# Kernel tuning notes

Measured on AMD Instinct MI355X. Metric: run time of the kernel, lower is better.

Reference implementation:

```python
import jax, jax.numpy as jnp
import numpy as np

IN_F = 512
OUT_F = 512
GRID_SIZE = 5
SPLINE_ORDER = 3
BATCH = 16384
GRID_MIN, GRID_MAX = -1.0, 1.0


def setup_inputs() -> dict:
    key = jax.random.key(0)
    k1, k2, k3 = jax.random.split(key, 3)
    x = jax.random.normal(k1, (BATCH, IN_F), dtype=jnp.float32)
    # kaiming-uniform-ish scale for base weight
    base_weight = jax.random.normal(k2, (OUT_F, IN_F), dtype=jnp.float32) * (1.0 / np.sqrt(IN_F))
    spline_weight = jax.random.normal(k3, (OUT_F, IN_F, GRID_SIZE + SPLINE_ORDER), dtype=jnp.float32) * 0.1
    spline_scaler = jnp.ones((OUT_F, IN_F), dtype=jnp.float32)  # init'd to scale_spline=1.0
    # grid buffer: (in_features, grid_size + 2*spline_order + 1)
    h = (GRID_MAX - GRID_MIN) / GRID_SIZE
    knots = jnp.arange(-SPLINE_ORDER, GRID_SIZE + SPLINE_ORDER + 1, dtype=jnp.float32) * h + GRID_MIN
    grid = jnp.broadcast_to(knots, (IN_F, GRID_SIZE + 2 * SPLINE_ORDER + 1))
    return {"x": x, "base_weight": base_weight, "spline_weight": spline_weight,
            "spline_scaler": spline_scaler, "grid": grid}


def _b_splines(x, grid):
    # x: (B, in), grid: (in, G + 2k + 1) -> bases: (B, in, G + k)
    xe = x[..., None]  # (B, in, 1)
    bases = ((xe >= grid[:, :-1]) & (xe < grid[:, 1:])).astype(x.dtype)
    for k in range(1, SPLINE_ORDER + 1):
        den1 = jnp.maximum(grid[:, k:-1] - grid[:, :-(k + 1)], 1e-6)
        den2 = jnp.maximum(grid[:, k + 1:] - grid[:, 1:-k], 1e-6)
        bases = ((xe - grid[:, :-(k + 1)]) / den1 * bases[..., :-1]
                 + (grid[:, k + 1:] - xe) / den2 * bases[..., 1:])
    return bases


def reference(x, base_weight, spline_weight, spline_scaler, grid):
    # _finite: nan_to_num + clamp to [-6, 6]
    x = jnp.clip(jnp.nan_to_num(x, nan=0.0, posinf=6.0, neginf=-6.0), -6.0, 6.0)
    # clamp to slightly outside grid range, then (identity-like) renormalize
    x = jnp.clip(x, GRID_MIN - 0.1, GRID_MAX + 0.1)
    x = (x - GRID_MIN) / (GRID_MAX - GRID_MIN + 1e-8) * (GRID_MAX - GRID_MIN) + GRID_MIN
    base_out = jax.nn.silu(x) @ base_weight.T  # (B, out)
    bases = _b_splines(x, grid)                # (B, in, G+k)
    scaled_sw = spline_weight * spline_scaler[..., None]  # (out, in, G+k)
    spline_out = jnp.einsum('big,oig->bo', bases, scaled_sw)
    y = base_out + spline_out
    return jnp.where(jnp.isfinite(y), y, jnp.zeros_like(y))
```

## Files before the change

kernel.cpp:

```cpp
#include <hip/hip_runtime.h>
#include <stdint.h>


#define IN_F   512
#define OUT_F  512
#define KDIM   4608
#define BATCH  16384

#define BM 128
#define BN 128
#define BKI 128
#define NT (KDIM / BKI)
#define A_I8 (BM * BKI)
#define TILE_I8 (2 * A_I8)

#define SSCALE 154.0f
#define BSCALE 190.5f

typedef unsigned char u8;
typedef int i32x4 __attribute__((ext_vector_type(4)));

__device__ __forceinline__ float cleanx(float v) {
    if (v != v) v = 0.0f;
    v = fminf(fmaxf(v, -6.0f), 6.0f);
    return fminf(fmaxf(v, -1.1f), 1.1f);
}

__global__ __launch_bounds__(256) void prep_w_kernel(const float* __restrict__ bw,
                                                     const float* __restrict__ sw,
                                                     const float* __restrict__ sc,
                                                     char* __restrict__ Wc,
                                                     float* __restrict__ EpiS) {
    const int o = blockIdx.x;
    const int t = threadIdx.x;
    const float* wbrow = bw + (size_t)o * IN_F;
    const float* wsrow = sw + (size_t)o * 4096;
    const float* srow  = sc + (size_t)o * IN_F;

    float vb0 = wbrow[t * 2], vb1 = wbrow[t * 2 + 1];
    float mxb = fmaxf(fabsf(vb0), fabsf(vb1));
    float vs[16];
    float mxs = 0.0f;
    #pragma unroll
    for (int e = 0; e < 16; ++e) {
        int k = t * 16 + e;
        float v = wsrow[k] * srow[k >> 3];
        vs[e] = v;
        mxs = fmaxf(mxs, fabsf(v));
    }
    #pragma unroll
    for (int off = 32; off >= 1; off >>= 1) {
        mxb = fmaxf(mxb, __shfl_xor(mxb, off));
        mxs = fmaxf(mxs, __shfl_xor(mxs, off));
    }
    __shared__ float wmx[8];
    if ((t & 63) == 0) { wmx[t >> 6] = mxb; wmx[4 + (t >> 6)] = mxs; }
    __syncthreads();
    float gb = fmaxf(fmaxf(wmx[0], wmx[1]), fmaxf(wmx[2], wmx[3]));
    float gs = fmaxf(fmaxf(wmx[4], wmx[5]), fmaxf(wmx[6], wmx[7]));
    float S = fminf(SSCALE * 127.0f / fmaxf(gb, 1e-20f),
                    BSCALE * 127.0f / fmaxf(gs, 1e-20f));
    if (t == 0) EpiS[o] = 1.0f / S;

    const int swz = (o & 7) << 4;
    float sb = S / SSCALE;
    char q0 = (char)__float2int_rn(fminf(fmaxf(vb0 * sb, -127.f), 127.f));
    char q1 = (char)__float2int_rn(fminf(fmaxf(vb1 * sb, -127.f), 127.f));
    union { char c[2]; short s; } p2; p2.c[0] = q0; p2.c[1] = q1;
    *reinterpret_cast<short*>(Wc + (size_t)o * KDIM + ((t * 2) ^ swz)) = p2.s;
    float ss = S / BSCALE;
    union { char q[16]; uint4 v; } pk;
    #pragma unroll
    for (int e = 0; e < 16; ++e) {
        float q = fminf(fmaxf(vs[e] * ss, -127.f), 127.f);
        pk.q[e] = (char)__float2int_rn(q);
    }
    *reinterpret_cast<uint4*>(Wc + (size_t)o * KDIM + ((512 + t * 16) ^ swz)) = pk.v;
}

__global__ void prep_x_kernel(const float* __restrict__ x,
                              char* __restrict__ Act) {
    int idx = blockIdx.x * 256 + threadIdx.x;
    int b  = idx >> 6;
    int g8 = idx & 63;
    const int swz = (b & 7) << 4;
    const float4* xp = reinterpret_cast<const float4*>(x + (size_t)b * IN_F + g8 * 8);
    float4 v0 = xp[0], v1 = xp[1];
    float vv[8] = {v0.x, v0.y, v0.z, v0.w, v1.x, v1.y, v1.z, v1.w};

    union { char q[8]; uint2 u; } sq;
    union { char q[64]; uint4 u[4]; } bq;
    #pragma unroll
    for (int e = 0; e < 8; ++e) {
        float v = cleanx(vv[e]);
        float s = v / (1.0f + __expf(-v));
        sq.q[e] = (char)__float2int_rn(s * SSCALE);

        float t = (v + 2.2f) * 2.5f;
        int m = (int)floorf(t);
        m = min(max(m, 2), 8);
        float u = t - (float)m;
        float u2 = u * u;
        float u3 = u2 * u;
        float p0 = u3 * (1.0f / 6.0f);
        float p1 = (1.0f + 3.0f * u + 3.0f * u2 - 3.0f * u3) * (1.0f / 6.0f);
        float p2 = (4.0f - 6.0f * u2 + 3.0f * u3) * (1.0f / 6.0f);
        float w1 = 1.0f - u;
        float p3 = w1 * w1 * w1 * (1.0f / 6.0f);
        #pragma unroll
        for (int g = 0; g < 8; ++g) {
            int j = m - g;
            float r = 0.0f;
            r = (j == 0) ? p0 : r;
            r = (j == 1) ? p1 : r;
            r = (j == 2) ? p2 : r;
            r = (j == 3) ? p3 : r;
            bq.q[e * 8 + g] = (char)(r * BSCALE + 0.5f);
        }
    }
    char* arow = Act + (size_t)b * KDIM;
    *reinterpret_cast<uint2*>(arow + ((g8 * 8) ^ swz)) = sq.u;
    const int k0 = 512 + g8 * 64;
    #pragma unroll
    for (int c = 0; c < 4; ++c)
        *reinterpret_cast<uint4*>(arow + ((k0 + c * 16) ^ swz)) = bq.u[c];
}

__global__ __launch_bounds__(256, 2) void gemm_kernel(const char* __restrict__ Act,
                                                      const char* __restrict__ Wc,
                                                      const float* __restrict__ EpiS,
                                                      float* __restrict__ C) {
    __shared__ __align__(16) u8 SmB[2 * TILE_I8];

    const int tid  = threadIdx.x;
    const int w    = tid >> 6;
    const int lane = tid & 63;

    const int bid = blockIdx.x;
    const int wg  = (bid & 7) * 64 + (bid >> 3);
    const int bm0 = (wg >> 2) * BM;
    const int bn0 = (wg & 3) * BN;

    const int wr = (w >> 1) * 64;
    const int wc = (w & 1) * 64;

    const int rA  = lane & 15;
    const int kg8 = (lane >> 4) * 16;

    i32x4 acc[4][4] = {};

    auto stage = [&](u8* dst, int kt) {
        #pragma unroll
        for (int c = 0; c < 4; ++c) {
            int off = tid * 16 + c * 4096;
            int row = off >> 7, col = off & 127;
            const char* ga = Act + (size_t)(bm0 + row) * KDIM + kt * BKI + col;
            const char* gb = Wc  + (size_t)(bn0 + row) * KDIM + kt * BKI + col;
            __builtin_amdgcn_global_load_lds(
                (const __attribute__((address_space(1))) uint32_t*)ga,
                (__attribute__((address_space(3))) uint32_t*)(dst + off), 16, 0, 0);
            __builtin_amdgcn_global_load_lds(
                (const __attribute__((address_space(1))) uint32_t*)gb,
                (__attribute__((address_space(3))) uint32_t*)(dst + A_I8 + off), 16, 0, 0);
        }
    };

    stage(SmB, 0);
    int cur = 0;
    for (int t = 0; t < NT; ++t) {
        __builtin_amdgcn_s_barrier();
        if (t + 1 < NT) {
            stage(SmB + (cur ^ 1) * TILE_I8, t + 1);
            asm volatile("s_waitcnt vmcnt(8)" ::: "memory");
        } else {
            asm volatile("s_waitcnt vmcnt(0)" ::: "memory");
        }
        __builtin_amdgcn_s_barrier();

        const u8* Aa = SmB + cur * TILE_I8;
        const u8* Bb = Aa + A_I8;

        i32x4 af[4][2], bfr[2][4];
        #pragma unroll
        for (int kk = 0; kk < 2; ++kk) {
            #pragma unroll
            for (int m = 0; m < 4; ++m) {
                const int row = wr + m * 16 + rA;
                const int col = (kk * 64 + kg8) ^ ((row & 7) << 4);
                af[m][kk] = *reinterpret_cast<const i32x4*>(&Aa[row * BKI + col]);
            }
            #pragma unroll
            for (int n = 0; n < 4; ++n) {
                const int row = wc + n * 16 + rA;
                const int col = (kk * 64 + kg8) ^ ((row & 7) << 4);
                bfr[kk][n] = *reinterpret_cast<const i32x4*>(&Bb[row * BKI + col]);
            }
        }
        __builtin_amdgcn_s_setprio(1);
        #pragma unroll
        for (int kk = 0; kk < 2; ++kk)
            #pragma unroll
            for (int m = 0; m < 4; ++m)
                #pragma unroll
                for (int n = 0; n < 4; ++n)
                    acc[m][n] = __builtin_amdgcn_mfma_i32_16x16x64_i8(
                        af[m][kk], bfr[kk][n], acc[m][n], 0, 0, 0);
        __builtin_amdgcn_s_setprio(0);
        cur ^= 1;
    }

    const int rq = lane >> 4;
    const int cn = lane & 15;
    #pragma unroll
    for (int n = 0; n < 4; ++n) {
        const int col = bn0 + wc + n * 16 + cn;
        const float es = EpiS[col];
        #pragma unroll
        for (int m = 0; m < 4; ++m) {
            const int row0 = bm0 + wr + m * 16 + rq * 4;
            float* cp = C + (size_t)row0 * OUT_F + col;
            cp[0 * OUT_F] = (float)acc[m][n][0] * es;
            cp[1 * OUT_F] = (float)acc[m][n][1] * es;
            cp[2 * OUT_F] = (float)acc[m][n][2] * es;
            cp[3 * OUT_F] = (float)acc[m][n][3] * es;
        }
    }
}

extern "C" void kernel_launch(void* const* d_in, const int* in_sizes, int n_in,
                              void* d_out, int out_size, void* d_ws, size_t ws_size,
                              hipStream_t stream) {
    const float* x  = (const float*)d_in[0];
    const float* bw = (const float*)d_in[1];
    const float* sw = (const float*)d_in[2];
    const float* sc = (const float*)d_in[3];

    char* p = (char*)d_ws;
    char*  Wc   = p;                   p += (size_t)OUT_F * KDIM;
    float* EpiS = (float*)p;           p += OUT_F * sizeof(float);
    char*  Act  = p;

    prep_w_kernel<<<OUT_F, 256, 0, stream>>>(bw, sw, sc, Wc, EpiS);
    prep_x_kernel<<<(BATCH * 64) / 256, 256, 0, stream>>>(x, Act);
    gemm_kernel<<<(BATCH / BM) * (OUT_F / BN), 256, 0, stream>>>(
        Act, Wc, EpiS, (float*)d_out);
}
```

Measured before the change: 77.92 us.

## Split K across warp pairs with LDS reduction instead of 2x2 warp tiling

The four waves are re-partitioned. Each wave now covers 128 rows by 64 columns over half of the K-slice of each tile, instead of a 64x64 quadrant over the full K-slice. This halves the LDS fragment loads per wave per tile: 12 16-byte reads instead of 16. The cost is twice the accumulator registers (128 ints per lane) and an end-of-kernel LDS reduction between wave pairs. The larger register footprint may threaten the 2-blocks-per-CU occupancy target.

```diff
diff --git a/kernel.cpp b/kernel.cpp
--- a/kernel.cpp
+++ b/kernel.cpp
@@ -141,13 +141,14 @@
     const int bm0 = (wg >> 2) * BM;
     const int bn0 = (wg & 3) * BN;
 
-    const int wr = (w >> 1) * 64;
-    const int wc = (w & 1) * 64;
+    const int wc = (w >> 1) * 64;
+    const int kh = w & 1;
 
     const int rA  = lane & 15;
     const int kg8 = (lane >> 4) * 16;
-
-    i32x4 acc[4][4] = {};
+    const int kcb = kh * 64 + kg8;
+
+    i32x4 acc[8][4] = {};
 
     auto stage = [&](u8* dst, int kt) {
         #pragma unroll
@@ -180,49 +181,58 @@
         const u8* Aa = SmB + cur * TILE_I8;
         const u8* Bb = Aa + A_I8;
 
-        i32x4 af[4][2], bfr[2][4];
-        #pragma unroll
-        for (int kk = 0; kk < 2; ++kk) {
+        i32x4 af[8], bfr[4];
+        #pragma unroll
+        for (int m = 0; m < 8; ++m) {
+            const int row = m * 16 + rA;
+            af[m] = *reinterpret_cast<const i32x4*>(&Aa[row * BKI + (kcb ^ ((row & 7) << 4))]);
+        }
+        #pragma unroll
+        for (int n = 0; n < 4; ++n) {
+            const int row = wc + n * 16 + rA;
+            bfr[n] = *reinterpret_cast<const i32x4*>(&Bb[row * BKI + (kcb ^ ((row & 7) << 4))]);
+        }
+
+        __builtin_amdgcn_s_setprio(1);
+        #pragma unroll
+        for (int m = 0; m < 8; ++m)
             #pragma unroll
-            for (int m = 0; m < 4; ++m) {
-                const int row = wr + m * 16 + rA;
-                const int col = (kk * 64 + kg8) ^ ((row & 7) << 4);
-                af[m][kk] = *reinterpret_cast<const i32x4*>(&Aa[row * BKI + col]);
-            }
-            #pragma unroll
-            for (int n = 0; n < 4; ++n) {
-                const int row = wc + n * 16 + rA;
-                const int col = (kk * 64 + kg8) ^ ((row & 7) << 4);
-                bfr[kk][n] = *reinterpret_cast<const i32x4*>(&Bb[row * BKI + col]);
-            }
-        }
-        __builtin_amdgcn_s_setprio(1);
-        #pragma unroll
-        for (int kk = 0; kk < 2; ++kk)
-            #pragma unroll
-            for (int m = 0; m < 4; ++m)
-                #pragma unroll
-                for (int n = 0; n < 4; ++n)
-                    acc[m][n] = __builtin_amdgcn_mfma_i32_16x16x64_i8(
-                        af[m][kk], bfr[kk][n], acc[m][n], 0, 0, 0);
+            for (int n = 0; n < 4; ++n)
+                acc[m][n] = __builtin_amdgcn_mfma_i32_16x16x64_i8(
+                    af[m], bfr[n], acc[m][n], 0, 0, 0);
         __builtin_amdgcn_s_setprio(0);
         cur ^= 1;
     }
 
-    const int rq = lane >> 4;
-    const int cn = lane & 15;
-    #pragma unroll
-    for (int n = 0; n < 4; ++n) {
-        const int col = bn0 + wc + n * 16 + cn;
-        const float es = EpiS[col];
-        #pragma unroll
-        for (int m = 0; m < 4; ++m) {
-            const int row0 = bm0 + wr + m * 16 + rq * 4;
-            float* cp = C + (size_t)row0 * OUT_F + col;
-            cp[0 * OUT_F] = (float)acc[m][n][0] * es;
-            cp[1 * OUT_F] = (float)acc[m][n][1] * es;
-            cp[2 * OUT_F] = (float)acc[m][n][2] * es;
-            cp[3 * OUT_F] = (float)acc[m][n][3] * es;
+    __builtin_amdgcn_s_barrier();
+    int* red = reinterpret_cast<int*>(SmB);
+    const int half = (w >> 1) * 8192;
+    if (kh == 1) {
+        #pragma unroll
+        for (int m = 0; m < 8; ++m)
+            #pragma unroll
+            for (int n = 0; n < 4; ++n)
+                *reinterpret_cast<i32x4*>(&red[half + ((m * 4 + n) * 64 + lane) * 4]) = acc[m][n];
+    }
+    __builtin_amdgcn_s_barrier();
+
+    if (kh == 0) {
+        const int rq = lane >> 4;
+        const int cn = lane & 15;
+        #pragma unroll
+        for (int n = 0; n < 4; ++n) {
+            const int col = bn0 + wc + n * 16 + cn;
+            const float es = EpiS[col];
+            #pragma unroll
+            for (int m = 0; m < 8; ++m) {
+                i32x4 o = *reinterpret_cast<const i32x4*>(&red[half + ((m * 4 + n) * 64 + lane) * 4]);
+                const int row0 = bm0 + m * 16 + rq * 4;
+                float* cp = C + (size_t)row0 * OUT_F + col;
+                cp[0 * OUT_F] = (float)(acc[m][n][0] + o[0]) * es;
+                cp[1 * OUT_F] = (float)(acc[m][n][1] + o[1]) * es;
+                cp[2 * OUT_F] = (float)(acc[m][n][2] + o[2]) * es;
+                cp[3 * OUT_F] = (float)(acc[m][n][3] + o[3]) * es;
+            }
         }
     }
 }
```

New measurement: 79.10 us. No clear change (+1.5%).

## Fuse activation quantization into GEMM and widen N tile to 256

Applied to the files above, without the earlier changes.

Removes the separate prep_x kernel and its int8 activation buffer. Each GEMM block now reads x directly, computes SiLU and cubic B-spline bases in registers, and writes the quantized A tile into LDS while the previous tile's MFMAs run. B tiles are still loaded with global_load_lds. The block grows to 512 threads with a 128x256 tile and one block per CU, so each x row is read and re-derived by only two column blocks. This saves the global round trip of the 75MB activation buffer, at the cost of redundant basis computation across blocks, lower occupancy and a full vmcnt(0) barrier every step.

```diff
diff --git a/kernel.cpp b/kernel.cpp
--- a/kernel.cpp
+++ b/kernel.cpp
@@ -8,11 +8,12 @@
 #define BATCH  16384
 
 #define BM 128
-#define BN 128
+#define BN 256
 #define BKI 128
-#define NT (KDIM / BKI)
-#define A_I8 (BM * BKI)
-#define TILE_I8 (2 * A_I8)
+#define NT 36
+#define A_T (BM * BKI)
+#define B_T (BN * BKI)
+#define LDS_BYTES (2 * A_T + 2 * B_T)
 
 #define SSCALE 154.0f
 #define BSCALE 190.5f
@@ -78,122 +79,122 @@
     *reinterpret_cast<uint4*>(Wc + (size_t)o * KDIM + ((512 + t * 16) ^ swz)) = pk.v;
 }
 
-__global__ void prep_x_kernel(const float* __restrict__ x,
-                              char* __restrict__ Act) {
-    int idx = blockIdx.x * 256 + threadIdx.x;
-    int b  = idx >> 6;
-    int g8 = idx & 63;
-    const int swz = (b & 7) << 4;
-    const float4* xp = reinterpret_cast<const float4*>(x + (size_t)b * IN_F + g8 * 8);
-    float4 v0 = xp[0], v1 = xp[1];
-    float vv[8] = {v0.x, v0.y, v0.z, v0.w, v1.x, v1.y, v1.z, v1.w};
-
-    union { char q[8]; uint2 u; } sq;
-    union { char q[64]; uint4 u[4]; } bq;
-    #pragma unroll
-    for (int e = 0; e < 8; ++e) {
-        float v = cleanx(vv[e]);
-        float s = v / (1.0f + __expf(-v));
-        sq.q[e] = (char)__float2int_rn(s * SSCALE);
-
-        float t = (v + 2.2f) * 2.5f;
-        int m = (int)floorf(t);
-        m = min(max(m, 2), 8);
-        float u = t - (float)m;
-        float u2 = u * u;
-        float u3 = u2 * u;
-        float p0 = u3 * (1.0f / 6.0f);
-        float p1 = (1.0f + 3.0f * u + 3.0f * u2 - 3.0f * u3) * (1.0f / 6.0f);
-        float p2 = (4.0f - 6.0f * u2 + 3.0f * u3) * (1.0f / 6.0f);
-        float w1 = 1.0f - u;
-        float p3 = w1 * w1 * w1 * (1.0f / 6.0f);
-        #pragma unroll
-        for (int g = 0; g < 8; ++g) {
-            int j = m - g;
-            float r = 0.0f;
-            r = (j == 0) ? p0 : r;
-            r = (j == 1) ? p1 : r;
-            r = (j == 2) ? p2 : r;
-            r = (j == 3) ? p3 : r;
-            bq.q[e * 8 + g] = (char)(r * BSCALE + 0.5f);
-        }
-    }
-    char* arow = Act + (size_t)b * KDIM;
-    *reinterpret_cast<uint2*>(arow + ((g8 * 8) ^ swz)) = sq.u;
-    const int k0 = 512 + g8 * 64;
-    #pragma unroll
-    for (int c = 0; c < 4; ++c)
-        *reinterpret_cast<uint4*>(arow + ((k0 + c * 16) ^ swz)) = bq.u[c];
-}
-
-__global__ __launch_bounds__(256, 2) void gemm_kernel(const char* __restrict__ Act,
-                                                      const char* __restrict__ Wc,
-                                                      const float* __restrict__ EpiS,
-                                                      float* __restrict__ C) {
-    __shared__ __align__(16) u8 SmB[2 * TILE_I8];
-
+extern __shared__ u8 Sm[];
+
+__global__ __launch_bounds__(512, 1) void kan_kernel(const float* __restrict__ x,
+                                                     const char* __restrict__ Wc,
+                                                     const float* __restrict__ EpiS,
+                                                     float* __restrict__ C) {
     const int tid  = threadIdx.x;
     const int w    = tid >> 6;
     const int lane = tid & 63;
 
     const int bid = blockIdx.x;
-    const int wg  = (bid & 7) * 64 + (bid >> 3);
-    const int bm0 = (wg >> 2) * BM;
-    const int bn0 = (wg & 3) * BN;
-
-    const int wr = (w >> 1) * 64;
-    const int wc = (w & 1) * 64;
+    const int wg  = (bid & 7) * 32 + (bid >> 3);
+    const int bm0 = (wg >> 1) * BM;
+    const int bn0 = (wg & 1) * BN;
+
+    const int wr = (w >> 2) * 64;
+    const int wcc = (w & 3) * 64;
 
     const int rA  = lane & 15;
     const int kg8 = (lane >> 4) * 16;
 
+    u8* Ar[2] = { Sm, Sm + A_T };
+    u8* Br[2] = { Sm + 2 * A_T, Sm + 2 * A_T + B_T };
+
+    const int pr = tid >> 2;
+    const int ps = tid & 3;
+    const uint32_t wswz = (uint32_t)((pr & 7) << 4);
+    const float* xrow = x + (size_t)(bm0 + pr) * IN_F;
+
     i32x4 acc[4][4] = {};
 
-    auto stage = [&](u8* dst, int kt) {
+    auto stageB = [&](u8* dst, int kt) {
         #pragma unroll
         for (int c = 0; c < 4; ++c) {
-            int off = tid * 16 + c * 4096;
+            int off = tid * 16 + c * 8192;
             int row = off >> 7, col = off & 127;
-            const char* ga = Act + (size_t)(bm0 + row) * KDIM + kt * BKI + col;
-            const char* gb = Wc  + (size_t)(bn0 + row) * KDIM + kt * BKI + col;
+            const char* g = Wc + (size_t)(bn0 + row) * KDIM + kt * BKI + col;
             __builtin_amdgcn_global_load_lds(
-                (const __attribute__((address_space(1))) uint32_t*)ga,
+                (const __attribute__((address_space(1))) uint32_t*)g,
                 (__attribute__((address_space(3))) uint32_t*)(dst + off), 16, 0, 0);
-            __builtin_amdgcn_global_load_lds(
-                (const __attribute__((address_space(1))) uint32_t*)gb,
-                (__attribute__((address_space(3))) uint32_t*)(dst + A_I8 + off), 16, 0, 0);
-        }
-    };
-
-    stage(SmB, 0);
-    int cur = 0;
-    for (int t = 0; t < NT; ++t) {
-        __builtin_amdgcn_s_barrier();
-        if (t + 1 < NT) {
-            stage(SmB + (cur ^ 1) * TILE_I8, t + 1);
-            asm volatile("s_waitcnt vmcnt(8)" ::: "memory");
-        } else {
-            asm volatile("s_waitcnt vmcnt(0)" ::: "memory");
-        }
-        __builtin_amdgcn_s_barrier();
-
-        const u8* Aa = SmB + cur * TILE_I8;
-        const u8* Bb = Aa + A_I8;
-
+        }
+    };
+
+    auto load_silu = [&](float4 (&S)[8], int tt) {
+        #pragma unroll
+        for (int j = 0; j < 8; ++j)
+            S[j] = *reinterpret_cast<const float4*>(xrow + tt * 128 + ps * 32 + j * 4);
+    };
+
+    auto produce_silu = [&](u8* dst, const float4 (&S)[8]) {
+        union { char c[16]; uint4 v; } pk0, pk1;
+        #pragma unroll
+        for (int j = 0; j < 8; ++j) {
+            float vv[4] = {S[j].x, S[j].y, S[j].z, S[j].w};
+            #pragma unroll
+            for (int e = 0; e < 4; ++e) {
+                float v = cleanx(vv[e]);
+                float s = v / (1.0f + __expf(-v));
+                char q = (char)__float2int_rn(s * SSCALE);
+                if (j < 4) pk0.c[j * 4 + e] = q; else pk1.c[(j - 4) * 4 + e] = q;
+            }
+        }
+        *reinterpret_cast<uint4*>(dst + pr * BKI + ((ps * 32)      ^ wswz)) = pk0.v;
+        *reinterpret_cast<uint4*>(dst + pr * BKI + ((ps * 32 + 16) ^ wswz)) = pk1.v;
+    };
+
+    auto produce_bases = [&](u8* dst, float4 xq) {
+        uint32_t wd[8];
+        float vv[4] = {xq.x, xq.y, xq.z, xq.w};
+        #pragma unroll
+        for (int e = 0; e < 4; ++e) {
+            float v = cleanx(vv[e]);
+            float t = (v + 2.2f) * 2.5f;
+            int mm = (int)floorf(t);
+            mm = min(max(mm, 2), 8);
+            float u = t - (float)mm;
+            float u2 = u * u, u3 = u2 * u;
+            float p0 = u3 * (1.0f / 6.0f);
+            float p1 = (1.0f + 3.0f * u + 3.0f * u2 - 3.0f * u3) * (1.0f / 6.0f);
+            float pq = (4.0f - 6.0f * u2 + 3.0f * u3) * (1.0f / 6.0f);
+            float w1 = 1.0f - u;
+            float p3 = w1 * w1 * w1 * (1.0f / 6.0f);
+            uint32_t q0 = (uint32_t)(int)(p0 * BSCALE + 0.5f);
+            uint32_t q1 = (uint32_t)(int)(p1 * BSCALE + 0.5f);
+            uint32_t q2 = (uint32_t)(int)(pq * BSCALE + 0.5f);
+            uint32_t q3 = (uint32_t)(int)(p3 * BSCALE + 0.5f);
+            uint64_t V = (uint64_t)((q0 << 24) | (q1 << 16) | (q2 << 8) | q3);
+            V = (mm >= 3) ? (V << (8 * (mm - 3))) : (V >> 8);
+            wd[e * 2]     = (uint32_t)V;
+            wd[e * 2 + 1] = (uint32_t)(V >> 32);
+        }
+        uint4 a = {wd[0], wd[1], wd[2], wd[3]};
+        uint4 b = {wd[4], wd[5], wd[6], wd[7]};
+        *reinterpret_cast<uint4*>(dst + pr * BKI + ((ps * 32)      ^ wswz)) = a;
+        *reinterpret_cast<uint4*>(dst + pr * BKI + ((ps * 32 + 16) ^ wswz)) = b;
+    };
+
+    auto load_bases = [&](float4& q, int tt) {
+        q = *reinterpret_cast<const float4*>(xrow + (tt * 16 - 64) + ps * 4);
+    };
+
+    auto do_tile = [&](const u8* Aa, const u8* Bb) {
         i32x4 af[4][2], bfr[2][4];
         #pragma unroll
         for (int kk = 0; kk < 2; ++kk) {
             #pragma unroll
             for (int m = 0; m < 4; ++m) {
                 const int row = wr + m * 16 + rA;
-                const int col = (kk * 64 + kg8) ^ ((row & 7) << 4);
-                af[m][kk] = *reinterpret_cast<const i32x4*>(&Aa[row * BKI + col]);
+                af[m][kk] = *reinterpret_cast<const i32x4*>(
+                    &Aa[row * BKI + ((kk * 64 + kg8) ^ ((row & 7) << 4))]);
             }
             #pragma unroll
             for (int n = 0; n < 4; ++n) {
-                const int row = wc + n * 16 + rA;
-                const int col = (kk * 64 + kg8) ^ ((row & 7) << 4);
-                bfr[kk][n] = *reinterpret_cast<const i32x4*>(&Bb[row * BKI + col]);
+                const int row = wcc + n * 16 + rA;
+                bfr[kk][n] = *reinterpret_cast<const i32x4*>(
+                    &Bb[row * BKI + ((kk * 64 + kg8) ^ ((row & 7) << 4))]);
             }
         }
         __builtin_amdgcn_s_setprio(1);
@@ -206,14 +207,48 @@
                     acc[m][n] = __builtin_amdgcn_mfma_i32_16x16x64_i8(
                         af[m][kk], bfr[kk][n], acc[m][n], 0, 0, 0);
         __builtin_amdgcn_s_setprio(0);
-        cur ^= 1;
-    }
+    };
+
+#define TOP() do { \
+    asm volatile("s_waitcnt vmcnt(0) lgkmcnt(0)" ::: "memory"); \
+    __builtin_amdgcn_s_barrier(); } while (0)
+
+    float4 S0[8], S1[8];
+    float4 xqA, xqB;
+
+    load_silu(S0, 0);
+    asm volatile("s_waitcnt vmcnt(0)" ::: "memory");
+    produce_silu(Ar[0], S0);
+    load_silu(S1, 1);
+    stageB(Br[0], 0);
+
+    TOP(); stageB(Br[1], 1); load_silu(S0, 2);
+    do_tile(Ar[0], Br[0]); produce_silu(Ar[1], S1);
+    TOP(); stageB(Br[0], 2); load_silu(S1, 3);
+    do_tile(Ar[1], Br[1]); produce_silu(Ar[0], S0);
+    TOP(); stageB(Br[1], 3); load_bases(xqA, 4);
+    do_tile(Ar[0], Br[0]); produce_silu(Ar[1], S1);
+    TOP(); stageB(Br[0], 4); load_bases(xqB, 5);
+    do_tile(Ar[1], Br[1]); produce_bases(Ar[0], xqA);
+
+    for (int t = 4; t < 34; t += 2) {
+        TOP(); stageB(Br[(t + 1) & 1], t + 1); load_bases(xqA, t + 2);
+        do_tile(Ar[t & 1], Br[t & 1]); produce_bases(Ar[(t + 1) & 1], xqB);
+
+        TOP(); stageB(Br[t & 1], t + 2); load_bases(xqB, t + 3);
+        do_tile(Ar[(t + 1) & 1], Br[(t + 1) & 1]); produce_bases(Ar[t & 1], xqA);
+    }
+    TOP(); stageB(Br[1], 35);
+    do_tile(Ar[0], Br[0]); produce_bases(Ar[1], xqB);
+    TOP();
+    do_tile(Ar[1], Br[1]);
+#undef TOP
 
     const int rq = lane >> 4;
     const int cn = lane & 15;
     #pragma unroll
     for (int n = 0; n < 4; ++n) {
-        const int col = bn0 + wc + n * 16 + cn;
+        const int col = bn0 + wcc + n * 16 + cn;
         const float es = EpiS[col];
         #pragma unroll
         for (int m = 0; m < 4; ++m) {
@@ -237,11 +272,12 @@
 
     char* p = (char*)d_ws;
     char*  Wc   = p;                   p += (size_t)OUT_F * KDIM;
-    float* EpiS = (float*)p;           p += OUT_F * sizeof(float);
-    char*  Act  = p;
+    float* EpiS = (float*)p;
+
+    hipFuncSetAttribute((const void*)kan_kernel,
+                        hipFuncAttributeMaxDynamicSharedMemorySize, LDS_BYTES);
 
     prep_w_kernel<<<OUT_F, 256, 0, stream>>>(bw, sw, sc, Wc, EpiS);
-    prep_x_kernel<<<(BATCH * 64) / 256, 256, 0, stream>>>(x, Act);
-    gemm_kernel<<<(BATCH / BM) * (OUT_F / BN), 256, 0, stream>>>(
-        Act, Wc, EpiS, (float*)d_out);
-}
+    kan_kernel<<<(BATCH / BM) * (OUT_F / BN), 512, LDS_BYTES, stream>>>(
+        x, Wc, EpiS, (float*)d_out);
+}
```

Result: faster. 70.53 us (-9.5%).
